# Performance work log

Hardware: AMD Instinct MI355X
Metric: run time of the kernel (lower is better)

The kernel has to match this reference:

```python
import jax, jax.numpy as jnp
import numpy as np

N_HEAD = 16
N_EMBED = 2048


def setup_inputs() -> dict:
    key = jax.random.key(0)
    k1, k2, k3, k4, k5 = jax.random.split(key, 5)
    B, T, C = 4, 2048, N_EMBED
    scale = 1.0 / np.sqrt(C)
    return {
        "x": jax.random.normal(k1, (B, T, C), dtype=jnp.float32),
        "w_attn": jax.random.normal(k2, (C, 3 * C), dtype=jnp.float32) * scale,
        "b_attn": jnp.zeros((3 * C,), dtype=jnp.float32),
        "w_proj": jax.random.normal(k3, (C, C), dtype=jnp.float32) * scale,
        "b_proj": jnp.zeros((C,), dtype=jnp.float32),
    }


def reference(x, w_attn, b_attn, w_proj, b_proj):
    B, T, C = x.shape
    H = N_HEAD
    hd = C // H
    # fused QKV projection: [B,T,3C]
    qkv = jnp.einsum("btc,cd->btd", x, w_attn) + b_attn
    q, k, v = jnp.split(qkv, 3, axis=-1)
    # [B,H,T,hd]
    q = q.reshape(B, T, H, hd).transpose(0, 2, 1, 3)
    k = k.reshape(B, T, H, hd).transpose(0, 2, 1, 3)
    v = v.reshape(B, T, H, hd).transpose(0, 2, 1, 3)
    # scaled dot-product attention (no mask, no dropout at eval)
    scores = jnp.einsum("bhqd,bhkd->bhqk", q, k) / jnp.sqrt(jnp.asarray(hd, dtype=q.dtype))
    attn = jax.nn.softmax(scores, axis=-1)
    y = jnp.einsum("bhqk,bhkd->bhqd", attn, v)
    y = y.transpose(0, 2, 1, 3).reshape(B, T, C)
    return jnp.einsum("btc,cd->btd", y, w_proj) + b_proj
```

## Files before the change

kernel.cpp:

```cpp
#include <hip/hip_runtime.h>
#include <hip/hip_fp16.h>

typedef _Float16 f16;
typedef _Float16 half8 __attribute__((ext_vector_type(8)));
typedef float f32x4 __attribute__((ext_vector_type(4)));

#define NBAT 4
#define NT   2048
#define NC   2048
#define NHEAD 16
#define HD   128
#define NM   8192
#define N3C  6144
#define QK_LD 4096
#define ATT_SCALE 0.088388347648318447f

static __device__ __forceinline__ void gload16(const void* g, void* l) {
  __builtin_amdgcn_global_load_lds(
      (const __attribute__((address_space(1))) unsigned int*)g,
      (__attribute__((address_space(3))) unsigned int*)l, 16, 0, 0);
}


__global__ __launch_bounds__(256) void cvt_x_f16(const float* __restrict__ in,
                                                 f16* __restrict__ out) {
  size_t i = ((size_t)blockIdx.x * 256 + threadIdx.x) * 8;
  float4 a = *(const float4*)(in + i);
  float4 b = *(const float4*)(in + i + 4);
  half8 o;
  o[0] = (f16)a.x; o[1] = (f16)a.y; o[2] = (f16)a.z; o[3] = (f16)a.w;
  o[4] = (f16)b.x; o[5] = (f16)b.y; o[6] = (f16)b.z; o[7] = (f16)b.w;
  *(half8*)(out + i) = o;
}

__global__ __launch_bounds__(256) void cvt_tr_f16(const float* __restrict__ in,
                                                  f16* __restrict__ out,
                                                  int R, int CC) {
  __shared__ float tile[32][33];
  int cb = blockIdx.x * 32, rb = blockIdx.y * 32;
  int lx = threadIdx.x & 31, ly = threadIdx.x >> 5;
  for (int i = 0; i < 32; i += 8)
    tile[ly + i][lx] = in[(size_t)(rb + ly + i) * CC + cb + lx];
  __syncthreads();
  for (int i = 0; i < 32; i += 8)
    out[(size_t)(cb + ly + i) * R + rb + lx] = (f16)tile[lx][ly + i];
}

template <int OUTMODE>
__global__ __launch_bounds__(256, 2)
void gemm_bt(const f16* __restrict__ A, const f16* __restrict__ BT,
             const float* __restrict__ bias,
             f16* __restrict__ oqk, f16* __restrict__ ovT,
             float* __restrict__ of32, int M, int N, int K) {
  __shared__ f16 As[128 * 32];
  __shared__ f16 Bs[128 * 32];
  const int tid = threadIdx.x;
  const int w = tid >> 6, lane = tid & 63;
  const int lr = lane & 15, lg = lane >> 4;
  const int wm = w >> 1, wn = w & 1;
  const int bm = blockIdx.y, bn = blockIdx.x;

  const int srow = lane >> 2;
  const int skoff = (lane & 3) * 8;

  const f16* asrc[2];
  const f16* bsrc[2];
  for (int t = 0; t < 2; ++t) {
    int idx = w * 2 + t;
    asrc[t] = A + (size_t)(bm * 128 + idx * 16 + srow) * K + skoff;
    bsrc[t] = BT + (size_t)(bn * 128 + idx * 16 + srow) * K + skoff;
  }

  f32x4 acc[4][4] = {};

  for (int kt = 0; kt < K; kt += 32) {
    for (int t = 0; t < 2; ++t) {
      int idx = w * 2 + t;
      gload16(asrc[t] + kt, (void*)(As + idx * 512));
      gload16(bsrc[t] + kt, (void*)(Bs + idx * 512));
    }
    __syncthreads();
    half8 af[4], bf[4];
    for (int mi = 0; mi < 4; ++mi)
      af[mi] = *(const half8*)(As + (wm * 64 + mi * 16 + lr) * 32 + lg * 8);
    for (int ni = 0; ni < 4; ++ni)
      bf[ni] = *(const half8*)(Bs + (wn * 64 + ni * 16 + lr) * 32 + lg * 8);
    for (int mi = 0; mi < 4; ++mi)
      for (int ni = 0; ni < 4; ++ni)
        acc[mi][ni] = __builtin_amdgcn_mfma_f32_16x16x32_f16(
            af[mi], bf[ni], acc[mi][ni], 0, 0, 0);
    __syncthreads();
  }

  for (int ni = 0; ni < 4; ++ni) {
    int col = bn * 128 + wn * 64 + ni * 16 + lr;
    float bv = bias[col];
    for (int mi = 0; mi < 4; ++mi) {
      int row0 = bm * 128 + wm * 64 + mi * 16 + lg * 4;
      f32x4 v = acc[mi][ni];
      for (int r = 0; r < 4; ++r) {
        float val = v[r] + bv;
        int row = row0 + r;
        if (OUTMODE == 0) {
          of32[(size_t)row * N + col] = val;
        } else {
          if (col < 4096) {
            oqk[(size_t)row * QK_LD + col] = (f16)val;
          } else {
            int dfull = col - 4096;
            int hh = dfull >> 7, dd = dfull & 127;
            int bb = row >> 11, tt = row & 2047;
            ovT[((size_t)(bb * NHEAD + hh) * HD + dd) * NT + tt] = (f16)val;
          }
        }
      }
    }
  }
}

__global__ __launch_bounds__(256, 2)
void attn_fwd(const f16* __restrict__ qk, const f16* __restrict__ vT,
              f16* __restrict__ y) {
  const int bid = blockIdx.x;
  const int sid = (bid & 7) * 128 + (bid >> 3);
  const int qt = sid & 15;
  const int bh = sid >> 4;
  const int b = bh >> 4, h = bh & 15;
  const int tid = threadIdx.x, w = tid >> 6, lane = tid & 63;
  const int lr = lane & 15, lg = lane >> 4;

  __shared__ f16 Ks[2][64 * 128];
  __shared__ f16 Vs[2][128 * 64];
  __shared__ f16 Ps[4][2][16 * 64];

  half8 qf[2][4];
  for (int s = 0; s < 2; ++s) {
    const f16* qp = qk + (size_t)(b * NT + qt * 128 + w * 32 + s * 16 + lr) * QK_LD +
                    h * HD + lg * 8;
    for (int dc = 0; dc < 4; ++dc) qf[s][dc] = *(const half8*)(qp + dc * 32);
  }

  f32x4 accy[2][8] = {};
  f32x4 lacc[2] = {};
  float mrow[2][4];
  for (int s = 0; s < 2; ++s)
    for (int r = 0; r < 4; ++r) mrow[s][r] = -1e30f;

  half8 onev;
  for (int j = 0; j < 8; ++j) onev[j] = (f16)1.0f;

  const char* kbase[4];
  const char* vbase[4];
  for (int j = 0; j < 4; ++j) {
    int idx = w * 4 + j;
    {
      int row = idx * 4 + lg;
      int swz = (lr * 16) ^ ((row & 7) << 4);
      kbase[j] = (const char*)qk +
                 ((size_t)(b * NT + row) * QK_LD + 2048 + h * HD) * 2 + swz;
    }
    {
      int d = idx * 8 + (lane >> 3);
      int cj = (lane & 7) ^ (d & 7);
      vbase[j] = (const char*)vT + ((size_t)(bh * HD + d) * NT + cj * 8) * 2;
    }
  }

  for (int j = 0; j < 4; ++j) {
    int idx = w * 4 + j;
    gload16(kbase[j], (void*)((char*)Ks[0] + idx * 1024));
    gload16(vbase[j], (void*)((char*)Vs[0] + idx * 1024));
  }
  __syncthreads();

  int cur = 0;
  for (int kt = 0; kt < 32; ++kt) {
    if (kt + 1 < 32) {
      for (int j = 0; j < 4; ++j) {
        int idx = w * 4 + j;
        gload16(kbase[j] + (size_t)(kt + 1) * (64 * QK_LD * 2),
                (void*)((char*)Ks[cur ^ 1] + idx * 1024));
        gload16(vbase[j] + (size_t)(kt + 1) * 128,
                (void*)((char*)Vs[cur ^ 1] + idx * 1024));
      }
    }

    f32x4 sa[2][4] = {};
    for (int nb = 0; nb < 4; ++nb) {
      int kvr = nb * 16 + lr;
      const char* kr = (const char*)Ks[cur] + kvr * 256;
      int s7 = (kvr & 7) << 4;
      for (int dc = 0; dc < 4; ++dc) {
        half8 kb = *(const half8*)(kr + ((dc * 64 + lg * 16) ^ s7));
        sa[0][nb] = __builtin_amdgcn_mfma_f32_16x16x32_f16(qf[0][dc], kb, sa[0][nb], 0, 0, 0);
        sa[1][nb] = __builtin_amdgcn_mfma_f32_16x16x32_f16(qf[1][dc], kb, sa[1][nb], 0, 0, 0);
      }
    }

    for (int s = 0; s < 2; ++s) {
      float sv[4][4];
      float pml[4] = {-1e30f, -1e30f, -1e30f, -1e30f};
      for (int nb = 0; nb < 4; ++nb)
        for (int r = 0; r < 4; ++r) {
          float x = sa[s][nb][r] * ATT_SCALE;
          sv[nb][r] = x;
          pml[r] = fmaxf(pml[r], x);
        }
      bool ok = true;
      for (int r = 0; r < 4; ++r) ok &= (pml[r] <= mrow[s][r] + 8.0f);
      if (!__all(ok)) {
        for (int r = 0; r < 4; ++r) {
          for (int off = 1; off < 16; off <<= 1)
            pml[r] = fmaxf(pml[r], __shfl_xor(pml[r], off));
          float mn = fmaxf(mrow[s][r], pml[r]);
          float al = __expf(mrow[s][r] - mn);
          mrow[s][r] = mn;
          lacc[s][r] *= al;
          for (int db = 0; db < 8; ++db) accy[s][db][r] *= al;
        }
      }
      for (int nb = 0; nb < 4; ++nb)
        for (int r = 0; r < 4; ++r) {
          float p = __expf(sv[nb][r] - mrow[s][r]);
          int prow = lg * 4 + r;
          int chunk = (nb * 2 + (lr >> 3)) ^ (prow & 7);
          Ps[w][s][prow * 64 + chunk * 8 + (lr & 7)] = (f16)p;
        }
    }

    half8 pa[2][2];
    for (int s = 0; s < 2; ++s)
      for (int kc = 0; kc < 2; ++kc) {
        int chunk = (kc * 4 + lg) ^ (lr & 7);
        pa[s][kc] = *(const half8*)(&Ps[w][s][lr * 64 + chunk * 8]);
      }
    for (int s = 0; s < 2; ++s)
      for (int kc = 0; kc < 2; ++kc)
        lacc[s] = __builtin_amdgcn_mfma_f32_16x16x32_f16(pa[s][kc], onev, lacc[s], 0, 0, 0);

    for (int db = 0; db < 8; ++db) {
      int d = db * 16 + lr;
      const char* vr = (const char*)Vs[cur] + d * 128;
      int d7 = d & 7;
      for (int kc = 0; kc < 2; ++kc) {
        half8 vb = *(const half8*)(vr + (((kc * 4 + lg) ^ d7) * 16));
        accy[0][db] = __builtin_amdgcn_mfma_f32_16x16x32_f16(pa[0][kc], vb, accy[0][db], 0, 0, 0);
        accy[1][db] = __builtin_amdgcn_mfma_f32_16x16x32_f16(pa[1][kc], vb, accy[1][db], 0, 0, 0);
      }
    }

    __syncthreads();
    cur ^= 1;
  }

  for (int s = 0; s < 2; ++s) {
    f32x4 inv;
    for (int r = 0; r < 4; ++r) inv[r] = 1.0f / lacc[s][r];
    f16* yp = y + (size_t)(b * NT + qt * 128 + w * 32 + s * 16 + lg * 4) * NC +
              h * HD + lr;
    for (int db = 0; db < 8; ++db)
      for (int r = 0; r < 4; ++r)
        yp[(size_t)r * NC + db * 16] = (f16)(accy[s][db][r] * inv[r]);
  }
}

extern "C" void kernel_launch(void* const* d_in, const int* in_sizes, int n_in,
                              void* d_out, int out_size, void* d_ws, size_t ws_size,
                              hipStream_t stream) {
  (void)in_sizes; (void)n_in; (void)out_size; (void)ws_size;
  const float* x      = (const float*)d_in[0];
  const float* w_attn = (const float*)d_in[1];
  const float* b_attn = (const float*)d_in[2];
  const float* w_proj = (const float*)d_in[3];
  const float* b_proj = (const float*)d_in[4];
  float* out = (float*)d_out;

  char* p = (char*)d_ws;
  f16* xh  = (f16*)p; p += (size_t)NM * NC * 2;
  f16* waT = (f16*)p; p += (size_t)N3C * NC * 2;
  f16* wpT = (f16*)p; p += (size_t)NC * NC * 2;
  f16* qkb = (f16*)p; p += (size_t)NM * QK_LD * 2;
  f16* vT  = (f16*)p; p += (size_t)NBAT * NHEAD * HD * NT * 2;
  f16* yh  = (f16*)p; p += (size_t)NM * NC * 2;

  cvt_x_f16<<<8192, 256, 0, stream>>>(x, xh);
  cvt_tr_f16<<<dim3(192, 64), 256, 0, stream>>>(w_attn, waT, NC, N3C);
  cvt_tr_f16<<<dim3(64, 64), 256, 0, stream>>>(w_proj, wpT, NC, NC);
  gemm_bt<1><<<dim3(48, 64), 256, 0, stream>>>(xh, waT, b_attn, qkb, vT, nullptr,
                                               NM, N3C, NC);
  attn_fwd<<<1024, 256, 0, stream>>>(qkb, vT, yh);
  gemm_bt<0><<<dim3(16, 64), 256, 0, stream>>>(yh, wpT, b_proj, nullptr, nullptr,
                                               out, NM, NC, NC);
}
```

Before: 565.4 us.

## Replace GEMM with 256x256 double-buffered swizzled-LDS tile kernel

Replaces the 128x128, K=32 single-buffered GEMM with a 256x256 tile, K=64, 512-thread kernel. It double-buffers LDS loads through global_load_lds with partial vmcnt waits, XOR-swizzles the LDS layout to avoid bank conflicts, and remaps block IDs so neighbouring blocks share data in cache. The aim is more reuse per loaded byte and overlap of loads with MFMA work. The cost is 128KB of LDS per block, which limits occupancy, and more accumulator registers per thread.

```diff
diff --git a/kernel.cpp b/kernel.cpp
--- a/kernel.cpp
+++ b/kernel.cpp
@@ -47,70 +47,103 @@
 }
 
 template <int OUTMODE>
-__global__ __launch_bounds__(256, 2)
-void gemm_bt(const f16* __restrict__ A, const f16* __restrict__ BT,
+__global__ __launch_bounds__(512, 2)
+void gemm256(const f16* __restrict__ A, const f16* __restrict__ BT,
              const float* __restrict__ bias,
              f16* __restrict__ oqk, f16* __restrict__ ovT,
-             float* __restrict__ of32, int M, int N, int K) {
-  __shared__ f16 As[128 * 32];
-  __shared__ f16 Bs[128 * 32];
+             float* __restrict__ of32, int N, int K, int nbn) {
+  __shared__ f16 sA[2][256 * 64];
+  __shared__ f16 sB[2][256 * 64];
+
   const int tid = threadIdx.x;
-  const int w = tid >> 6, lane = tid & 63;
+  const int wv = tid >> 6, lane = tid & 63;
   const int lr = lane & 15, lg = lane >> 4;
-  const int wm = w >> 1, wn = w & 1;
-  const int bm = blockIdx.y, bn = blockIdx.x;
-
-  const int srow = lane >> 2;
-  const int skoff = (lane & 3) * 8;
-
-  const f16* asrc[2];
-  const f16* bsrc[2];
-  for (int t = 0; t < 2; ++t) {
-    int idx = w * 2 + t;
-    asrc[t] = A + (size_t)(bm * 128 + idx * 16 + srow) * K + skoff;
-    bsrc[t] = BT + (size_t)(bn * 128 + idx * 16 + srow) * K + skoff;
-  }
-
-  f32x4 acc[4][4] = {};
-
-  for (int kt = 0; kt < K; kt += 32) {
-    for (int t = 0; t < 2; ++t) {
-      int idx = w * 2 + t;
-      gload16(asrc[t] + kt, (void*)(As + idx * 512));
-      gload16(bsrc[t] + kt, (void*)(Bs + idx * 512));
-    }
-    __syncthreads();
-    half8 af[4], bf[4];
-    for (int mi = 0; mi < 4; ++mi)
-      af[mi] = *(const half8*)(As + (wm * 64 + mi * 16 + lr) * 32 + lg * 8);
-    for (int ni = 0; ni < 4; ++ni)
-      bf[ni] = *(const half8*)(Bs + (wn * 64 + ni * 16 + lr) * 32 + lg * 8);
-    for (int mi = 0; mi < 4; ++mi)
-      for (int ni = 0; ni < 4; ++ni)
-        acc[mi][ni] = __builtin_amdgcn_mfma_f32_16x16x32_f16(
-            af[mi], bf[ni], acc[mi][ni], 0, 0, 0);
-    __syncthreads();
-  }
-
-  for (int ni = 0; ni < 4; ++ni) {
-    int col = bn * 128 + wn * 64 + ni * 16 + lr;
-    float bv = bias[col];
-    for (int mi = 0; mi < 4; ++mi) {
-      int row0 = bm * 128 + wm * 64 + mi * 16 + lg * 4;
-      f32x4 v = acc[mi][ni];
-      for (int r = 0; r < 4; ++r) {
-        float val = v[r] + bv;
-        int row = row0 + r;
-        if (OUTMODE == 0) {
-          of32[(size_t)row * N + col] = val;
+  const int wm = wv >> 2, wn = wv & 3;
+
+  const int q8 = gridDim.x >> 3;
+  const int sid = ((int)blockIdx.x & 7) * q8 + ((int)blockIdx.x >> 3);
+  const int bm = sid / nbn, bn = sid % nbn;
+
+  const int srow = lane >> 3;
+  const int schk = (lane & 7) ^ srow;
+  const f16* aS = A + (size_t)(bm * 256 + wv * 8 + srow) * K + schk * 8;
+  const f16* bS = BT + (size_t)(bn * 256 + wv * 8 + srow) * K + schk * 8;
+  const size_t jstep = (size_t)64 * K;
+
+  const int NKT = K >> 6;
+  f32x4 acc[8][4] = {};
+
+#pragma unroll
+  for (int j = 0; j < 4; ++j) {
+    gload16(aS + j * jstep, (void*)(sA[0] + (j * 512 + wv * 64) * 8));
+    gload16(bS + j * jstep, (void*)(sB[0] + (j * 512 + wv * 64) * 8));
+  }
+
+  for (int kt = 0; kt < NKT; ++kt) {
+    const int c = kt & 1;
+    if (kt + 1 < NKT) {
+      const f16* aN = aS + (size_t)(kt + 1) * 64;
+      const f16* bN = bS + (size_t)(kt + 1) * 64;
+#pragma unroll
+      for (int j = 0; j < 4; ++j) {
+        gload16(aN + j * jstep, (void*)(sA[c ^ 1] + (j * 512 + wv * 64) * 8));
+        gload16(bN + j * jstep, (void*)(sB[c ^ 1] + (j * 512 + wv * 64) * 8));
+      }
+      asm volatile("s_waitcnt vmcnt(8)" ::: "memory");
+    } else {
+      asm volatile("s_waitcnt vmcnt(0)" ::: "memory");
+    }
+    __builtin_amdgcn_s_barrier();
+    asm volatile("" ::: "memory");
+
+    const f16* pa = sA[c] + (wm * 128 + lr) * 64;
+    const f16* pb = sB[c] + (wn * 64 + lr) * 64;
+#pragma unroll
+    for (int ks = 0; ks < 2; ++ks) {
+      const int xc = ((ks * 4 + lg) ^ (lr & 7)) * 8;
+      half8 a[8], b[4];
+#pragma unroll
+      for (int mf = 0; mf < 8; ++mf)
+        a[mf] = *(const half8*)(pa + mf * (16 * 64) + xc);
+#pragma unroll
+      for (int nf = 0; nf < 4; ++nf)
+        b[nf] = *(const half8*)(pb + nf * (16 * 64) + xc);
+#pragma unroll
+      for (int mf = 0; mf < 8; ++mf)
+#pragma unroll
+        for (int nf = 0; nf < 4; ++nf)
+          acc[mf][nf] = __builtin_amdgcn_mfma_f32_16x16x32_f16(
+              a[mf], b[nf], acc[mf][nf], 0, 0, 0);
+    }
+    asm volatile("" ::: "memory");
+    __builtin_amdgcn_s_barrier();
+  }
+
+#pragma unroll
+  for (int nf = 0; nf < 4; ++nf) {
+    const int col = bn * 256 + wn * 64 + nf * 16 + lr;
+    const float bv = bias[col];
+#pragma unroll
+    for (int mf = 0; mf < 8; ++mf) {
+      const int row0 = bm * 256 + wm * 128 + mf * 16 + lg * 4;
+      f32x4 v = acc[mf][nf];
+      if (OUTMODE == 0) {
+#pragma unroll
+        for (int r = 0; r < 4; ++r)
+          of32[(size_t)(row0 + r) * N + col] = v[r] + bv;
+      } else {
+        if (col < 4096) {
+#pragma unroll
+          for (int r = 0; r < 4; ++r)
+            oqk[(size_t)(row0 + r) * QK_LD + col] = (f16)(v[r] + bv);
         } else {
-          if (col < 4096) {
-            oqk[(size_t)row * QK_LD + col] = (f16)val;
-          } else {
-            int dfull = col - 4096;
-            int hh = dfull >> 7, dd = dfull & 127;
-            int bb = row >> 11, tt = row & 2047;
-            ovT[((size_t)(bb * NHEAD + hh) * HD + dd) * NT + tt] = (f16)val;
+          const int dfull = col - 4096;
+          const int hh = dfull >> 7, dd = dfull & 127;
+#pragma unroll
+          for (int r = 0; r < 4; ++r) {
+            const int row = row0 + r;
+            const int bb = row >> 11, tt = row & 2047;
+            ovT[((size_t)(bb * NHEAD + hh) * HD + dd) * NT + tt] = (f16)(v[r] + bv);
           }
         }
       }
@@ -286,9 +319,9 @@
   cvt_x_f16<<<8192, 256, 0, stream>>>(x, xh);
   cvt_tr_f16<<<dim3(192, 64), 256, 0, stream>>>(w_attn, waT, NC, N3C);
   cvt_tr_f16<<<dim3(64, 64), 256, 0, stream>>>(w_proj, wpT, NC, NC);
-  gemm_bt<1><<<dim3(48, 64), 256, 0, stream>>>(xh, waT, b_attn, qkb, vT, nullptr,
-                                               NM, N3C, NC);
+  gemm256<1><<<768, 512, 0, stream>>>(xh, waT, b_attn, qkb, vT, nullptr,
+                                      N3C, NC, 24);
   attn_fwd<<<1024, 256, 0, stream>>>(qkb, vT, yh);
-  gemm_bt<0><<<dim3(16, 64), 256, 0, stream>>>(yh, wpT, b_proj, nullptr, nullptr,
-                                               out, NM, NC, NC);
-}
+  gemm256<0><<<256, 512, 0, stream>>>(yh, wpT, b_proj, nullptr, nullptr,
+                                      out, NC, NC, 8);
+}
```

Measured after the change: 496.9 us. -12.1%, faster.
